# Performance work log

Measured on AMD Instinct MI355X. Metric: run time of the kernel, lower is better.

## Reference

```python
import jax, jax.numpy as jnp
import numpy as np

N, E, IN, HID, HEADS, L = 50000, 640000, 32, 64, 2, 4
MAXR = 8
N_ETYPE = 11 + 3 * MAXR  # 35
NEG_SLOPE = 0.2  # DGL EGATConv leaky_relu slope


def _mlp2(x, W1, b1, W2, b2):
    # 2-layer MLP: activation (gelu) after hidden layer only
    return jax.nn.gelu(x @ W1 + b1) @ W2 + b2


def _egat(h, ef, src, dst, W_ni, W_nj, W_fij, W_node, b_node, attn):
    # DGL EGATConv: edge-feature-enhanced graph attention
    n = h.shape[0]
    H, D = attn.shape
    f_edge = (h @ W_ni)[src] + (h @ W_nj)[dst] + ef @ W_fij       # [E, H*D]
    f_out = jax.nn.leaky_relu(f_edge, NEG_SLOPE).reshape(-1, H, D)
    e = jnp.einsum('ehd,hd->eh', f_out, attn)                     # [E, H]
    m = jax.ops.segment_max(e, dst, num_segments=n)               # per-dst max
    w = jnp.exp(e - m[dst])
    z = jax.ops.segment_sum(w, dst, num_segments=n)
    a = w / z[dst]                                                # edge softmax over incoming edges
    h_out = (h @ W_node + b_node).reshape(n, H, D)
    return jax.ops.segment_sum(h_out[src] * a[:, :, None], dst, num_segments=n)  # [N, H, D]


def _forward(feat, att_rc, att_rp, type_emb, rid_emb, rc_W, rc_b, rp_W, rp_b,
             fe_W1, fe_b1, fe_W2, fe_b2, W_ni, W_nj, W_fij, W_node, b_node, attn,
             mlp_W1, mlp_b1, mlp_W2, mlp_b2, src, dst, etype, erid):
    n = feat.shape[0]
    # edge embedding, 'sum' flavor
    ef = type_emb[etype] + rid_emb[erid] + att_rc @ rc_W + rc_b + att_rp @ rp_W + rp_b
    feats = [feat]
    h = _mlp2(feat, fe_W1, fe_b1, fe_W2, fe_b2)
    feats.append(h)
    for l in range(W_ni.shape[0]):
        agg = _egat(h, ef, src, dst, W_ni[l], W_nj[l], W_fij[l],
                    W_node[l], b_node[l], attn[l])
        h = _mlp2(agg.reshape(n, -1), mlp_W1[l], mlp_b1[l], mlp_W2[l], mlp_b2[l]) + h  # residual
        feats.append(h)
    node_emb = jnp.concatenate(feats, axis=-1)             # layer_pooling='all'
    graph_emb = jnp.max(node_emb, axis=0, keepdims=True)   # graph max pooling
    return jnp.concatenate([node_emb, jnp.broadcast_to(graph_emb, node_emb.shape)], axis=-1)


def setup_inputs() -> dict:
    key = jax.random.key(0)
    ks = iter(jax.random.split(key, 40))
    s = 0.05
    return {
        'feat': jax.random.normal(next(ks), (N, IN), jnp.float32),
        'att_rc': jax.random.normal(next(ks), (E, 2), jnp.float32),
        'att_rp': jax.random.normal(next(ks), (E, 3), jnp.float32),
        'type_emb': jax.random.normal(next(ks), (N_ETYPE, HID), jnp.float32) * s,
        'rid_emb': jax.random.normal(next(ks), (MAXR + 1, HID), jnp.float32) * s,
        'rc_W': jax.random.normal(next(ks), (2, HID), jnp.float32) * s,
        'rc_b': jnp.zeros((HID,), jnp.float32),
        'rp_W': jax.random.normal(next(ks), (3, HID), jnp.float32) * s,
        'rp_b': jnp.zeros((HID,), jnp.float32),
        'fe_W1': jax.random.normal(next(ks), (IN, HID), jnp.float32) * s,
        'fe_b1': jnp.zeros((HID,), jnp.float32),
        'fe_W2': jax.random.normal(next(ks), (HID, HID), jnp.float32) * s,
        'fe_b2': jnp.zeros((HID,), jnp.float32),
        'W_ni': jax.random.normal(next(ks), (L, HID, HEADS * HID), jnp.float32) * s,
        'W_nj': jax.random.normal(next(ks), (L, HID, HEADS * HID), jnp.float32) * s,
        'W_fij': jax.random.normal(next(ks), (L, HID, HEADS * HID), jnp.float32) * s,
        'W_node': jax.random.normal(next(ks), (L, HID, HEADS * HID), jnp.float32) * s,
        'b_node': jnp.zeros((L, HEADS * HID), jnp.float32),
        'attn': jax.random.normal(next(ks), (L, HEADS, HID), jnp.float32) * s,
        'mlp_W1': jax.random.normal(next(ks), (L, HEADS * HID, HEADS * HID), jnp.float32) * s,
        'mlp_b1': jnp.zeros((L, HEADS * HID), jnp.float32),
        'mlp_W2': jax.random.normal(next(ks), (L, HEADS * HID, HID), jnp.float32) * s,
        'mlp_b2': jnp.zeros((L, HID), jnp.float32),
        'src': jax.random.randint(next(ks), (E,), 0, N, jnp.int32),
        'dst': jax.random.randint(next(ks), (E,), 0, N, jnp.int32),
        'etype': jax.random.randint(next(ks), (E,), 0, N_ETYPE, jnp.int32),
        'erid': jax.random.randint(next(ks), (E,), 0, MAXR + 1, jnp.int32),
    }


def reference(feat, att_rc, att_rp, type_emb, rid_emb, rc_W, rc_b, rp_W, rp_b,
              fe_W1, fe_b1, fe_W2, fe_b2, W_ni, W_nj, W_fij, W_node, b_node, attn,
              mlp_W1, mlp_b1, mlp_W2, mlp_b2, src, dst, etype, erid):
    return _forward(feat, att_rc, att_rp, type_emb, rid_emb, rc_W, rc_b, rp_W, rp_b,
                    fe_W1, fe_b1, fe_W2, fe_b2, W_ni, W_nj, W_fij, W_node, b_node, attn,
                    mlp_W1, mlp_b1, mlp_W2, mlp_b2, src, dst, etype, erid)
```

## Files before the change

### kernel.cpp

```cpp
#include <hip/hip_runtime.h>
#include <math.h>

#define N_NODES 50000
#define N_EDGES 640000
#define NLAYER  4
#define NPAD    50016

#define EDGE_BLOCKS 1000
#define EDGE_WAVES  4000

typedef unsigned short bf16_t;
typedef __attribute__((ext_vector_type(8))) short s16x8;
typedef __attribute__((ext_vector_type(4))) float f32x4;

__device__ __forceinline__ float gelu_f(float x) {
    return 0.5f * x * (1.0f + tanhf(0.7978845608028654f * (x + 0.044715f * x * x * x)));
}

__device__ __forceinline__ bf16_t f2bf(float f) {
    unsigned u = __float_as_uint(f);
    unsigned r = (u + 0x7FFFu + ((u >> 16) & 1u)) >> 16;
    return (bf16_t)r;
}
__device__ __forceinline__ float bf2f(bf16_t h) { return __uint_as_float(((unsigned)h) << 16); }
__device__ __forceinline__ float bfl(unsigned x) { return __uint_as_float(x << 16); }
__device__ __forceinline__ float bfh(unsigned x) { return __uint_as_float(x & 0xFFFF0000u); }

__global__ void k_zero32(unsigned* p, int n) {
    int i = blockIdx.x * 256 + threadIdx.x;
    if (i < n) p[i] = 0u;
}

__global__ void k_hist(const int* __restrict__ dst, int* __restrict__ deg) {
    int i = blockIdx.x * 256 + threadIdx.x;
    if (i < N_EDGES) atomicAdd(&deg[dst[i]], 1);
}

__global__ void k_scan1(const int* __restrict__ deg, int* __restrict__ rowptr, int* __restrict__ bsum) {
    __shared__ int sd[1024];
    int gi = blockIdx.x * 1024 + threadIdx.x;
    int v = (gi < N_NODES) ? deg[gi] : 0;
    sd[threadIdx.x] = v;
    __syncthreads();
    for (int off = 1; off < 1024; off <<= 1) {
        int t2 = (threadIdx.x >= (unsigned)off) ? sd[threadIdx.x - off] : 0;
        __syncthreads();
        sd[threadIdx.x] += t2;
        __syncthreads();
    }
    if (gi < N_NODES) rowptr[gi] = sd[threadIdx.x] - v;
    if (threadIdx.x == 1023) bsum[blockIdx.x] = sd[1023];
}

__global__ void k_scan2(const int* __restrict__ bsum, int* __restrict__ boff, int nb) {
    if (threadIdx.x == 0 && blockIdx.x == 0) {
        int run = 0;
        for (int b = 0; b < nb; b++) { boff[b] = run; run += bsum[b]; }
    }
}

__global__ void k_scan3(int* __restrict__ rowptr, const int* __restrict__ boff) {
    int gi = blockIdx.x * 1024 + threadIdx.x;
    if (gi < N_NODES) rowptr[gi] += boff[blockIdx.x];
    if (gi == 0) rowptr[N_NODES] = N_EDGES;
}

__global__ void k_copy(const int* __restrict__ a, int* __restrict__ b) {
    int i = blockIdx.x * 256 + threadIdx.x;
    if (i < N_NODES) b[i] = a[i];
}

__global__ void k_scatter(const int* __restrict__ dst, int* __restrict__ cursor, int* __restrict__ eidx) {
    int i = blockIdx.x * 256 + threadIdx.x;
    if (i < N_EDGES) {
        int p = atomicAdd(&cursor[dst[i]], 1);
        eidx[p] = i;
    }
}

__global__ void k_sortgather(
    const int* __restrict__ eidx, const int* __restrict__ src, const int* __restrict__ dst,
    const int* __restrict__ etype, const int* __restrict__ erid,
    const float* __restrict__ att_rc, const float* __restrict__ att_rp,
    int* __restrict__ src_s, uint4* __restrict__ emA, uint2* __restrict__ emB)
{
    int i = blockIdx.x * 256 + threadIdx.x;
    if (i < N_EDGES) {
        int e = eidx[i];
        int sv = src[e];
        src_s[i] = sv;
        uint4 a;
        a.x = (unsigned)sv;
        a.y = (unsigned)dst[e];
        a.z = (unsigned)(etype[e] * 9 + erid[e]);
        a.w = (unsigned)f2bf(att_rc[2 * e]) | ((unsigned)f2bf(att_rc[2 * e + 1]) << 16);
        uint2 b;
        b.x = (unsigned)f2bf(att_rp[3 * e]) | ((unsigned)f2bf(att_rp[3 * e + 1]) << 16);
        b.y = (unsigned)f2bf(att_rp[3 * e + 2]);
        emA[i] = a;
        emB[i] = b;
    }
}

__global__ void k_base(const float* __restrict__ type_emb, const float* __restrict__ rid_emb,
                       const float* __restrict__ rcb, const float* __restrict__ rpb,
                       float* __restrict__ base)
{
    int idx = blockIdx.x * 256 + threadIdx.x;
    if (idx >= 315 * 64) return;
    int c = idx >> 6, k = idx & 63;
    int et = c / 9, er = c % 9;
    base[idx] = type_emb[et * 64 + k] + rid_emb[er * 64 + k] + rcb[k] + rpb[k];
}

__global__ void k_wprep(const float* __restrict__ Wfij, const float* __restrict__ Wni,
                        const float* __restrict__ Wnj, const float* __restrict__ Wnode,
                        const float* __restrict__ W1, const float* __restrict__ W2,
                        bf16_t* __restrict__ WT, bf16_t* __restrict__ W3T,
                        bf16_t* __restrict__ W1T, bf16_t* __restrict__ W2T)
{
    int idx = blockIdx.x * 256 + threadIdx.x;
    if (idx >= NLAYER * 57344) return;
    int l = idx / 57344, r = idx % 57344;
    if (r < 8192) {
        int n = r >> 6, k = r & 63;
        WT[l * 8192 + r] = f2bf(Wfij[l * 8192 + k * 128 + n]);
    } else if (r < 32768) {
        int q = r - 8192; int c = q >> 6, k = q & 63;
        const float* src = (c < 128) ? Wni : (c < 256) ? Wnj : Wnode;
        W3T[l * 24576 + q] = f2bf(src[l * 8192 + k * 128 + (c & 127)]);
    } else if (r < 49152) {
        int q = r - 32768; int n = q >> 7, k = q & 127;
        W1T[l * 16384 + q] = f2bf(W1[l * 16384 + k * 128 + n]);
    } else {
        int q = r - 49152; int j = q >> 7, k = q & 127;
        W2T[l * 8192 + q] = f2bf(W2[l * 8192 + k * 64 + j]);
    }
}

__global__ __launch_bounds__(256) void k_fe(
    const float* __restrict__ feat, const float* __restrict__ W1, const float* __restrict__ b1,
    const float* __restrict__ W2, const float* __restrict__ b2,
    float* __restrict__ h, bf16_t* __restrict__ hb, float* __restrict__ out)
{
    __shared__ float hid[4][64];
    int w = threadIdx.x >> 6, lane = threadIdx.x & 63;
    int n = blockIdx.x * 4 + w;
    float a = b1[lane];
#pragma unroll 8
    for (int k = 0; k < 32; k++) a = fmaf(feat[n * 32 + k], W1[k * 64 + lane], a);
    hid[w][lane] = gelu_f(a);
    __syncthreads();
    float o = b2[lane];
#pragma unroll 8
    for (int k = 0; k < 64; k++) o = fmaf(hid[w][k], W2[k * 64 + lane], o);
    h[n * 64 + lane] = o;
    hb[n * 64 + lane] = f2bf(o);
    out[n * 704 + 32 + lane] = o;
    if (lane < 32) out[n * 704 + lane] = feat[n * 32 + lane];
}

__global__ __launch_bounds__(256) void k_node3(
    const bf16_t* __restrict__ hb, const bf16_t* __restrict__ W3T,
    const float* __restrict__ bnode, bf16_t* __restrict__ s)
{
    __shared__ __align__(16) bf16_t hbS[32 * 72];
    const int t = threadIdx.x;
    const int wave = t >> 6, lane = t & 63, l16 = lane & 15, quad = lane >> 4;
    const int n0 = blockIdx.x * 32;
    {
        int r = t >> 3, sg = t & 7;
        *(s16x8*)(hbS + r * 72 + sg * 8) = *(const s16x8*)(hb + (size_t)(n0 + r) * 64 + sg * 8);
    }
    __syncthreads();
    const int ng = wave & 1, ch = wave >> 1;
    const s16x8 B0 = *(const s16x8*)(hbS + (ng * 16 + l16) * 72 + quad * 8);
    const s16x8 B1 = *(const s16x8*)(hbS + (ng * 16 + l16) * 72 + 32 + quad * 8);
    const int node = n0 + ng * 16 + l16;
#pragma unroll
    for (int nt = 0; nt < 12; nt++) {
        int c0 = ch * 192 + nt * 16;
        const s16x8 A0 = *(const s16x8*)(W3T + (size_t)(c0 + l16) * 64 + quad * 8);
        const s16x8 A1 = *(const s16x8*)(W3T + (size_t)(c0 + l16) * 64 + 32 + quad * 8);
        f32x4 acc = {0.f, 0.f, 0.f, 0.f};
        acc = __builtin_amdgcn_mfma_f32_16x16x32_bf16(A0, B0, acc, 0, 0, 0);
        acc = __builtin_amdgcn_mfma_f32_16x16x32_bf16(A1, B1, acc, 0, 0, 0);
        int cb = c0 + quad * 4;
        float4 bv = make_float4(0.f, 0.f, 0.f, 0.f);
        if (cb >= 256) bv = *(const float4*)(bnode + cb - 256);
        ushort4 o;
        o.x = f2bf(acc[0] + bv.x);
        o.y = f2bf(acc[1] + bv.y);
        o.z = f2bf(acc[2] + bv.z);
        o.w = f2bf(acc[3] + bv.w);
        *(ushort4*)(s + (size_t)node * 384 + cb) = o;
    }
}

__device__ __forceinline__ void eg_issue(
    const bf16_t* __restrict__ s, const uint4& ma, int quad, ushort4 (&G)[8])
{
    const bf16_t* sr = s + (size_t)ma.x * 384;
    const bf16_t* dr = s + (size_t)ma.y * 384 + 128;
#pragma unroll
    for (int mt = 0; mt < 4; mt++) {
        const int d0 = mt * 16 + quad * 4;
        G[mt]     = *(const ushort4*)(sr + d0);
        G[4 + mt] = *(const ushort4*)(dr + d0);
    }
}

__device__ __forceinline__ void eg_process(
    int i, const uint4& ma, const uint2& mb, const ushort4 (&G)[8],
    const bf16_t* __restrict__ WTs, const float* __restrict__ attL,
    const float (*__restrict__ cwL)[64], const float* __restrict__ base,
    int lane, int quad, float* __restrict__ evals)
{
    const float rc0 = bfl(ma.w), rc1 = bfh(ma.w);
    const float rp0 = bfl(mb.x), rp1 = bfh(mb.x), rp2 = bfl(mb.y);
    const float* bp = base + (size_t)ma.z * 64;
    s16x8 B0, B1;
#pragma unroll
    for (int s4 = 0; s4 < 4; s4++) {
        const int k = (s4 >> 1) * 32 + (s4 & 1) * 4 + quad * 8;
        const float4 bv = *(const float4*)(bp + k);
        const float4 w0 = *(const float4*)(&cwL[0][k]);
        const float4 w1 = *(const float4*)(&cwL[1][k]);
        const float4 w2 = *(const float4*)(&cwL[2][k]);
        const float4 w3 = *(const float4*)(&cwL[3][k]);
        const float4 w4 = *(const float4*)(&cwL[4][k]);
        float v0 = bv.x, v1 = bv.y, v2 = bv.z, v3 = bv.w;
        v0 = fmaf(rc0, w0.x, v0); v1 = fmaf(rc0, w0.y, v1); v2 = fmaf(rc0, w0.z, v2); v3 = fmaf(rc0, w0.w, v3);
        v0 = fmaf(rc1, w1.x, v0); v1 = fmaf(rc1, w1.y, v1); v2 = fmaf(rc1, w1.z, v2); v3 = fmaf(rc1, w1.w, v3);
        v0 = fmaf(rp0, w2.x, v0); v1 = fmaf(rp0, w2.y, v1); v2 = fmaf(rp0, w2.z, v2); v3 = fmaf(rp0, w2.w, v3);
        v0 = fmaf(rp1, w3.x, v0); v1 = fmaf(rp1, w3.y, v1); v2 = fmaf(rp1, w3.z, v2); v3 = fmaf(rp1, w3.w, v3);
        v0 = fmaf(rp2, w4.x, v0); v1 = fmaf(rp2, w4.y, v1); v2 = fmaf(rp2, w4.z, v2); v3 = fmaf(rp2, w4.w, v3);
        const short p0 = (short)f2bf(v0), p1 = (short)f2bf(v1), p2 = (short)f2bf(v2), p3 = (short)f2bf(v3);
        const int o = (s4 & 1) * 4;
        if (s4 < 2) { B0[o] = p0; B0[o + 1] = p1; B0[o + 2] = p2; B0[o + 3] = p3; }
        else        { B1[o] = p0; B1[o + 1] = p1; B1[o + 2] = p2; B1[o + 3] = p3; }
    }
#pragma unroll
    for (int hd = 0; hd < 2; hd++) {
        float p = 0.f;
#pragma unroll
        for (int mt = 0; mt < 4; mt++) {
            const int fm = hd * 4 + mt;
            const s16x8 A0 = *(const s16x8*)(WTs + ((fm * 2 + 0) * 64 + lane) * 8);
            const s16x8 A1 = *(const s16x8*)(WTs + ((fm * 2 + 1) * 64 + lane) * 8);
            f32x4 a = {0.f, 0.f, 0.f, 0.f};
            a = __builtin_amdgcn_mfma_f32_16x16x32_bf16(A0, B0, a, 0, 0, 0);
            a = __builtin_amdgcn_mfma_f32_16x16x32_bf16(A1, B1, a, 0, 0, 0);
            const float4 at = *(const float4*)(attL + hd * 64 + mt * 16 + quad * 4);
            float f0 = a[0] + (bf2f(G[mt].x) + bf2f(G[4 + mt].x));
            float f1 = a[1] + (bf2f(G[mt].y) + bf2f(G[4 + mt].y));
            float f2 = a[2] + (bf2f(G[mt].z) + bf2f(G[4 + mt].z));
            float f3 = a[3] + (bf2f(G[mt].w) + bf2f(G[4 + mt].w));
            f0 = (f0 >= 0.f) ? f0 : 0.2f * f0;
            f1 = (f1 >= 0.f) ? f1 : 0.2f * f1;
            f2 = (f2 >= 0.f) ? f2 : 0.2f * f2;
            f3 = (f3 >= 0.f) ? f3 : 0.2f * f3;
            p = fmaf(f0, at.x, p);
            p = fmaf(f1, at.y, p);
            p = fmaf(f2, at.z, p);
            p = fmaf(f3, at.w, p);
        }
        p += __shfl_xor(p, 16);
        p += __shfl_xor(p, 32);
        if (quad == 0) evals[i * 2 + hd] = p;
    }
}

__global__ __launch_bounds__(256) void k_edge(
    const bf16_t* __restrict__ s, const bf16_t* __restrict__ WT,
    const float* __restrict__ attn, const uint4* __restrict__ emA,
    const uint2* __restrict__ emB, const float* __restrict__ base,
    const float* __restrict__ rcW, const float* __restrict__ rpW,
    float* __restrict__ evals)
{
    __shared__ __align__(16) bf16_t WTs[16 * 64 * 8];
    __shared__ __align__(16) float attL[128];
    __shared__ __align__(16) float cwL[5][64];
    for (int c = threadIdx.x; c < 1024; c += 256) {
        int ln = c & 63, rowq = c >> 6;
        int half = rowq & 1, fm = rowq >> 1;
        int rl16 = ln & 15, rq = ln >> 4;
        int grow = (fm >> 2) * 64 + (fm & 3) * 16 + rl16;
        *(s16x8*)(WTs + c * 8) = *(const s16x8*)(WT + grow * 64 + half * 32 + rq * 8);
    }
    if (threadIdx.x < 128) attL[threadIdx.x] = attn[threadIdx.x];
    {
        int j = threadIdx.x >> 6, k = threadIdx.x & 63;
        cwL[j][k] = (j < 2) ? rcW[j * 64 + k] : rpW[(j - 2) * 64 + k];
        if (threadIdx.x < 64) cwL[4][threadIdx.x] = rpW[128 + threadIdx.x];
    }
    __syncthreads();

    const int lane = threadIdx.x & 63;
    const int l16 = lane & 15, quad = lane >> 4;
    const int wid = (blockIdx.x * 256 + threadIdx.x) >> 6;

    ushort4 GA[8], GB[8];
    uint4 maC = emA[wid * 16 + l16];
    uint2 mbC = emB[wid * 16 + l16];
    eg_issue(s, maC, quad, GA);
    uint4 maN = emA[(wid + EDGE_WAVES) * 16 + l16];
    uint2 mbN = emB[(wid + EDGE_WAVES) * 16 + l16];

#pragma unroll 1
    for (int it = 0; it < 5; it++) {
        const int ta = wid + (2 * it) * EDGE_WAVES;
        const int tb = ta + EDGE_WAVES;
        eg_issue(s, maN, quad, GB);
        const bool h = it < 4;
        uint4 ma2 = maC; uint2 mb2 = mbC;
        if (h) {
            int e2 = (tb + EDGE_WAVES) * 16 + l16;
            ma2 = emA[e2]; mb2 = emB[e2];
        }
        eg_process(ta * 16 + l16, maC, mbC, GA, WTs, attL, cwL, base, lane, quad, evals);
        if (h) eg_issue(s, ma2, quad, GA);
        uint4 ma3 = maN; uint2 mb3 = mbN;
        if (h) {
            int e3 = (tb + 2 * EDGE_WAVES) * 16 + l16;
            ma3 = emA[e3]; mb3 = emB[e3];
        }
        eg_process(tb * 16 + l16, maN, mbN, GB, WTs, attL, cwL, base, lane, quad, evals);
        maC = ma2; mbC = mb2; maN = ma3; mbN = mb3;
    }
}

__global__ __launch_bounds__(256) void k_soft_agg(
    const int* __restrict__ rowptr, const int* __restrict__ src_s,
    const float* __restrict__ evals, const bf16_t* __restrict__ s,
    unsigned* __restrict__ aggb)
{
    int lane = threadIdx.x & 63;
    int wid = (blockIdx.x * 256 + threadIdx.x) >> 6;
    int nw = (gridDim.x * 256) >> 6;
    const int hb = (lane >> 4) & 1;
    const int esel = lane >> 5;
    const int s32 = (lane & 15) | ((lane >> 5) << 4);
    const int dsel = (lane & 31) * 4;
    for (int n = wid; n < N_NODES; n += nw) {
        int r0 = rowptr[n], r1 = rowptr[n + 1];
        if (r0 == r1) {
            if (lane < 32) { uint2 z; z.x = 0u; z.y = 0u; *(uint2*)(aggb + (size_t)n * 64 + lane * 2) = z; }
            continue;
        }
        float mm = -1e30f;
        for (int i = r0 + s32; i < r1; i += 32) mm = fmaxf(mm, evals[2 * i + hb]);
        mm = fmaxf(mm, __shfl_xor(mm, 1));
        mm = fmaxf(mm, __shfl_xor(mm, 2));
        mm = fmaxf(mm, __shfl_xor(mm, 4));
        mm = fmaxf(mm, __shfl_xor(mm, 8));
        mm = fmaxf(mm, __shfl_xor(mm, 32));
        float z = 0.f;
        for (int i = r0 + s32; i < r1; i += 32) z += expf(evals[2 * i + hb] - mm);
        z += __shfl_xor(z, 1);
        z += __shfl_xor(z, 2);
        z += __shfl_xor(z, 4);
        z += __shfl_xor(z, 8);
        z += __shfl_xor(z, 32);
        float rz = 1.f / z;
        float acc0 = 0.f, acc1 = 0.f, acc2 = 0.f, acc3 = 0.f;
        for (int i = r0; i < r1; i += 8) {
            uint2 cc[4]; float ww[4];
#pragma unroll
            for (int p = 0; p < 4; p++) {
                int ej = i + 2 * p + esel;
                bool v = ej < r1;
                int es = v ? ej : r0;
                cc[p] = *(const uint2*)(s + (size_t)src_s[es] * 384 + 256 + dsel);
                ww[p] = v ? expf(evals[2 * ej + hb] - mm) * rz : 0.f;
            }
#pragma unroll
            for (int p = 0; p < 4; p++) {
                acc0 = fmaf(ww[p], bfl(cc[p].x), acc0);
                acc1 = fmaf(ww[p], bfh(cc[p].x), acc1);
                acc2 = fmaf(ww[p], bfl(cc[p].y), acc2);
                acc3 = fmaf(ww[p], bfh(cc[p].y), acc3);
            }
        }
        acc0 += __shfl_xor(acc0, 32);
        acc1 += __shfl_xor(acc1, 32);
        acc2 += __shfl_xor(acc2, 32);
        acc3 += __shfl_xor(acc3, 32);
        if (lane < 32) {
            uint2 o;
            o.x = (unsigned)f2bf(acc0) | ((unsigned)f2bf(acc1) << 16);
            o.y = (unsigned)f2bf(acc2) | ((unsigned)f2bf(acc3) << 16);
            *(uint2*)(aggb + (size_t)n * 64 + lane * 2) = o;
        }
    }
}

__global__ __launch_bounds__(256) void k_mlp(
    const bf16_t* __restrict__ aggb, const bf16_t* __restrict__ W1T, const float* __restrict__ b1,
    const bf16_t* __restrict__ W2T, const float* __restrict__ b2,
    const float* __restrict__ hin, float* __restrict__ hout, bf16_t* __restrict__ houtb,
    float* __restrict__ out, int col0)
{
    __shared__ __align__(16) bf16_t aggS[32 * 136];
    __shared__ __align__(16) bf16_t hidS[32 * 136];
    const int t = threadIdx.x;
    const int wave = t >> 6, lane = t & 63, l16 = lane & 15, quad = lane >> 4;
    const int n0 = blockIdx.x * 32;
    {
        int r = t >> 3, sg = t & 7;
        *(s16x8*)(aggS + r * 136 + sg * 16) =
            *(const s16x8*)(aggb + (size_t)(n0 + r) * 128 + sg * 16);
        *(s16x8*)(aggS + r * 136 + sg * 16 + 8) =
            *(const s16x8*)(aggb + (size_t)(n0 + r) * 128 + sg * 16 + 8);
    }
    __syncthreads();
    const int ng = wave & 1, nh = wave >> 1;
    const int node = n0 + ng * 16 + l16;
    {
        const bf16_t* brow = aggS + (ng * 16 + l16) * 136 + quad * 8;
        s16x8 B[4];
#pragma unroll
        for (int ks = 0; ks < 4; ks++) B[ks] = *(const s16x8*)(brow + ks * 32);
#pragma unroll
        for (int nt = 0; nt < 4; nt++) {
            int nb = nh * 64 + nt * 16;
            f32x4 acc = {0.f, 0.f, 0.f, 0.f};
#pragma unroll
            for (int ks = 0; ks < 4; ks++) {
                const s16x8 A = *(const s16x8*)(W1T + (size_t)(nb + l16) * 128 + ks * 32 + quad * 8);
                acc = __builtin_amdgcn_mfma_f32_16x16x32_bf16(A, B[ks], acc, 0, 0, 0);
            }
            const float4 bv = *(const float4*)(b1 + nb + quad * 4);
            ushort4 o;
            o.x = f2bf(gelu_f(acc[0] + bv.x));
            o.y = f2bf(gelu_f(acc[1] + bv.y));
            o.z = f2bf(gelu_f(acc[2] + bv.z));
            o.w = f2bf(gelu_f(acc[3] + bv.w));
            *(ushort4*)(hidS + (ng * 16 + l16) * 136 + nb + quad * 4) = o;
        }
    }
    __syncthreads();
    {
        const int jh = wave >> 1;
        const bf16_t* hrow = hidS + (ng * 16 + l16) * 136 + quad * 8;
        s16x8 H[4];
#pragma unroll
        for (int ks = 0; ks < 4; ks++) H[ks] = *(const s16x8*)(hrow + ks * 32);
#pragma unroll
        for (int jt = 0; jt < 2; jt++) {
            int jb = jh * 32 + jt * 16;
            f32x4 acc = {0.f, 0.f, 0.f, 0.f};
#pragma unroll
            for (int ks = 0; ks < 4; ks++) {
                const s16x8 A = *(const s16x8*)(W2T + (size_t)(jb + l16) * 128 + ks * 32 + quad * 8);
                acc = __builtin_amdgcn_mfma_f32_16x16x32_bf16(A, H[ks], acc, 0, 0, 0);
            }
            int j0 = jb + quad * 4;
            const float4 bv = *(const float4*)(b2 + j0);
            const float4 hv = *(const float4*)(hin + (size_t)node * 64 + j0);
            float4 v;
            v.x = acc[0] + bv.x + hv.x;
            v.y = acc[1] + bv.y + hv.y;
            v.z = acc[2] + bv.z + hv.z;
            v.w = acc[3] + bv.w + hv.w;
            *(float4*)(hout + (size_t)node * 64 + j0) = v;
            ushort4 ob;
            ob.x = f2bf(v.x); ob.y = f2bf(v.y); ob.z = f2bf(v.z); ob.w = f2bf(v.w);
            *(ushort4*)(houtb + (size_t)node * 64 + j0) = ob;
            if (node < N_NODES)
                *(float4*)(out + (size_t)node * 704 + col0 + j0) = v;
        }
    }
}

__device__ __forceinline__ unsigned fmap(float v) {
    unsigned u = __float_as_uint(v);
    return (u & 0x80000000u) ? ~u : (u | 0x80000000u);
}

__global__ __launch_bounds__(384) void k_colmax(const float* __restrict__ out, unsigned* __restrict__ gmax) {
    int c = threadIdx.x;
    if (c >= 352) return;
    float m = -1e30f;
    for (int n = blockIdx.x; n < N_NODES; n += gridDim.x)
        m = fmaxf(m, out[(size_t)n * 704 + c]);
    atomicMax(gmax + c, fmap(m));
}

__global__ __launch_bounds__(384) void k_bcast(const unsigned* __restrict__ gmax, float* __restrict__ out) {
    int c = threadIdx.x;
    if (c >= 352) return;
    unsigned u = gmax[c];
    u = (u & 0x80000000u) ? (u ^ 0x80000000u) : ~u;
    float v = __uint_as_float(u);
    for (int n = blockIdx.x; n < N_NODES; n += gridDim.x)
        out[(size_t)n * 704 + 352 + c] = v;
}

extern "C" void kernel_launch(void* const* d_in, const int* in_sizes, int n_in,
                              void* d_out, int out_size, void* d_ws, size_t ws_size,
                              hipStream_t stream)
{
    (void)in_sizes; (void)n_in; (void)out_size; (void)ws_size;
    const float* feat     = (const float*)d_in[0];
    const float* att_rc   = (const float*)d_in[1];
    const float* att_rp   = (const float*)d_in[2];
    const float* type_emb = (const float*)d_in[3];
    const float* rid_emb  = (const float*)d_in[4];
    const float* rc_W     = (const float*)d_in[5];
    const float* rc_b     = (const float*)d_in[6];
    const float* rp_W     = (const float*)d_in[7];
    const float* rp_b     = (const float*)d_in[8];
    const float* fe_W1    = (const float*)d_in[9];
    const float* fe_b1    = (const float*)d_in[10];
    const float* fe_W2    = (const float*)d_in[11];
    const float* fe_b2    = (const float*)d_in[12];
    const float* W_ni     = (const float*)d_in[13];
    const float* W_nj     = (const float*)d_in[14];
    const float* W_fij    = (const float*)d_in[15];
    const float* W_node   = (const float*)d_in[16];
    const float* b_node   = (const float*)d_in[17];
    const float* attn     = (const float*)d_in[18];
    const float* mlp_W1   = (const float*)d_in[19];
    const float* mlp_b1   = (const float*)d_in[20];
    const float* mlp_W2   = (const float*)d_in[21];
    const float* mlp_b2   = (const float*)d_in[22];
    const int* src   = (const int*)d_in[23];
    const int* dst   = (const int*)d_in[24];
    const int* etype = (const int*)d_in[25];
    const int* erid  = (const int*)d_in[26];
    float* out = (float*)d_out;

    char* cur = (char*)d_ws;
    auto alloc = [&](size_t bytes) { char* p = cur; cur += (bytes + 15) & ~(size_t)15; return p; };
    float* h_a    = (float*)alloc((size_t)NPAD * 64 * 4);
    float* h_b    = (float*)alloc((size_t)NPAD * 64 * 4);
    bf16_t* hb_a  = (bf16_t*)alloc((size_t)NPAD * 64 * 2);
    bf16_t* hb_b  = (bf16_t*)alloc((size_t)NPAD * 64 * 2);
    bf16_t* s     = (bf16_t*)alloc((size_t)NPAD * 384 * 2);
    float* ev     = (float*)alloc((size_t)N_EDGES * 2 * 4);
    bf16_t* aggb  = (bf16_t*)alloc((size_t)NPAD * 128 * 2);
    int* deg     = (int*)alloc((size_t)N_NODES * 4);
    int* rowptr  = (int*)alloc((size_t)(N_NODES + 1) * 4);
    int* cursor  = (int*)alloc((size_t)N_NODES * 4);
    int* eidx    = (int*)alloc((size_t)N_EDGES * 4);
    int* src_s   = (int*)alloc((size_t)N_EDGES * 4);
    uint4* emA   = (uint4*)alloc((size_t)N_EDGES * 16);
    uint2* emB   = (uint2*)alloc((size_t)N_EDGES * 8);
    float* baseT = (float*)alloc((size_t)315 * 64 * 4);
    bf16_t* WT   = (bf16_t*)alloc((size_t)NLAYER * 128 * 64 * 2);
    bf16_t* W3T  = (bf16_t*)alloc((size_t)NLAYER * 384 * 64 * 2);
    bf16_t* W1T  = (bf16_t*)alloc((size_t)NLAYER * 128 * 128 * 2);
    bf16_t* W2T  = (bf16_t*)alloc((size_t)NLAYER * 64 * 128 * 2);
    int* bsum    = (int*)alloc(64 * 4);
    int* boff    = (int*)alloc(64 * 4);
    unsigned* gmax = (unsigned*)alloc(352 * 4);

    const int NB = (N_NODES + 1023) / 1024;

    k_zero32<<<(N_NODES + 255) / 256, 256, 0, stream>>>((unsigned*)deg, N_NODES);
    k_zero32<<<2, 256, 0, stream>>>(gmax, 352);
    k_hist<<<N_EDGES / 256, 256, 0, stream>>>(dst, deg);
    k_scan1<<<NB, 1024, 0, stream>>>(deg, rowptr, bsum);
    k_scan2<<<1, 64, 0, stream>>>(bsum, boff, NB);
    k_scan3<<<NB, 1024, 0, stream>>>(rowptr, boff);
    k_copy<<<(N_NODES + 255) / 256, 256, 0, stream>>>(rowptr, cursor);
    k_scatter<<<N_EDGES / 256, 256, 0, stream>>>(dst, cursor, eidx);
    k_sortgather<<<N_EDGES / 256, 256, 0, stream>>>(eidx, src, dst, etype, erid, att_rc, att_rp,
                                                    src_s, emA, emB);
    k_base<<<(315 * 64 + 255) / 256, 256, 0, stream>>>(type_emb, rid_emb, rc_b, rp_b, baseT);
    k_wprep<<<(NLAYER * 57344 + 255) / 256, 256, 0, stream>>>(
        W_fij, W_ni, W_nj, W_node, mlp_W1, mlp_W2, WT, W3T, W1T, W2T);
    k_fe<<<N_NODES / 4, 256, 0, stream>>>(feat, fe_W1, fe_b1, fe_W2, fe_b2, h_a, hb_a, out);

    float* hc = h_a;  bf16_t* hbc = hb_a;
    float* hn = h_b;  bf16_t* hbn = hb_b;
    for (int l = 0; l < NLAYER; l++) {
        k_node3<<<NPAD / 32, 256, 0, stream>>>(hbc, W3T + (size_t)l * 384 * 64, b_node + l * 128, s);
        k_edge<<<EDGE_BLOCKS, 256, 0, stream>>>(s, WT + l * 128 * 64, attn + l * 128,
                                                emA, emB, baseT, rc_W, rp_W, ev);
        k_soft_agg<<<4096, 256, 0, stream>>>(rowptr, src_s, ev, s, (unsigned*)aggb);
        k_mlp<<<NPAD / 32, 256, 0, stream>>>(aggb, W1T + (size_t)l * 128 * 128, mlp_b1 + l * 128,
                                             W2T + (size_t)l * 64 * 128, mlp_b2 + l * 64,
                                             hc, hn, hbn, out, 32 + 64 * (l + 1));
        float* tf = hc; hc = hn; hn = tf;
        bf16_t* tb = hbc; hbc = hbn; hbn = tb;
    }
    k_colmax<<<512, 384, 0, stream>>>(out, gmax);
    k_bcast<<<512, 384, 0, stream>>>(gmax, out);
}
```

Measured before the change: 1.258 ms.

## Precompute edge-feature projection tables and replace MFMA edge kernel with per-thread scalar path

The edge embedding is affine in a small categorical index and five scalar attributes. This change folds W_fij into a per-(type,rid) table and five per-attribute weight vectors, computed once per layer in small setup kernels, so the per-edge 64x128 matmul becomes a table lookup plus five FMAs per output. The edge kernel becomes one thread per edge with no shared memory or MFMA, replacing the software-pipelined wave-per-16-edges loop. The cost is more per-thread registers and scattered 16-byte gathers of 128-float table rows and bf16 node rows. Accumulating in fp32 instead of rounding edge features to bf16 also changes numerics slightly.

```diff
diff --git a/kernel.cpp b/kernel.cpp
--- a/kernel.cpp
+++ b/kernel.cpp
@@ -5,9 +5,6 @@
 #define N_EDGES 640000
 #define NLAYER  4
 #define NPAD    50016
-
-#define EDGE_BLOCKS 1000
-#define EDGE_WAVES  4000
 
 typedef unsigned short bf16_t;
 typedef __attribute__((ext_vector_type(8))) short s16x8;
@@ -111,6 +108,36 @@
     int c = idx >> 6, k = idx & 63;
     int et = c / 9, er = c % 9;
     base[idx] = type_emb[et * 64 + k] + rid_emb[er * 64 + k] + rcb[k] + rpb[k];
+}
+
+__global__ void k_basew(const float* __restrict__ base, const float* __restrict__ Wfij,
+                        float* __restrict__ baseW)
+{
+    int idx = blockIdx.x * 256 + threadIdx.x;
+    if (idx >= NLAYER * 315 * 128) return;
+    int l = idx / (315 * 128), r = idx % (315 * 128);
+    int c = r >> 7, n = r & 127;
+    const float* bp = base + c * 64;
+    const float* wp = Wfij + l * 8192 + n;
+    float acc = 0.f;
+#pragma unroll 8
+    for (int k = 0; k < 64; k++) acc = fmaf(bp[k], wp[k * 128], acc);
+    baseW[idx] = acc;
+}
+
+__global__ void k_cw(const float* __restrict__ rcW, const float* __restrict__ rpW,
+                     const float* __restrict__ Wfij, float* __restrict__ CWf)
+{
+    int idx = blockIdx.x * 256 + threadIdx.x;
+    if (idx >= NLAYER * 5 * 128) return;
+    int l = idx / 640, r = idx % 640;
+    int j = r >> 7, n = r & 127;
+    const float* cp = (j < 2) ? (rcW + j * 64) : (rpW + (j - 2) * 64);
+    const float* wp = Wfij + l * 8192 + n;
+    float acc = 0.f;
+#pragma unroll 8
+    for (int k = 0; k < 64; k++) acc = fmaf(cp[k], wp[k * 128], acc);
+    CWf[idx] = acc;
 }
 
 __global__ void k_wprep(const float* __restrict__ Wfij, const float* __restrict__ Wni,
@@ -197,137 +224,75 @@
     }
 }
 
-__device__ __forceinline__ void eg_issue(
-    const bf16_t* __restrict__ s, const uint4& ma, int quad, ushort4 (&G)[8])
-{
+__global__ __launch_bounds__(256) void k_edge(
+    const bf16_t* __restrict__ s, const float* __restrict__ baseW,
+    const float* __restrict__ CWf, const float* __restrict__ attn,
+    const uint4* __restrict__ emA, const uint2* __restrict__ emB,
+    float* __restrict__ evals)
+{
+    const int i = blockIdx.x * 256 + threadIdx.x;
+    const uint4 ma = emA[i];
+    const uint2 mb = emB[i];
     const bf16_t* sr = s + (size_t)ma.x * 384;
     const bf16_t* dr = s + (size_t)ma.y * 384 + 128;
-#pragma unroll
-    for (int mt = 0; mt < 4; mt++) {
-        const int d0 = mt * 16 + quad * 4;
-        G[mt]     = *(const ushort4*)(sr + d0);
-        G[4 + mt] = *(const ushort4*)(dr + d0);
-    }
-}
-
-__device__ __forceinline__ void eg_process(
-    int i, const uint4& ma, const uint2& mb, const ushort4 (&G)[8],
-    const bf16_t* __restrict__ WTs, const float* __restrict__ attL,
-    const float (*__restrict__ cwL)[64], const float* __restrict__ base,
-    int lane, int quad, float* __restrict__ evals)
-{
-    const float rc0 = bfl(ma.w), rc1 = bfh(ma.w);
-    const float rp0 = bfl(mb.x), rp1 = bfh(mb.x), rp2 = bfl(mb.y);
-    const float* bp = base + (size_t)ma.z * 64;
-    s16x8 B0, B1;
-#pragma unroll
-    for (int s4 = 0; s4 < 4; s4++) {
-        const int k = (s4 >> 1) * 32 + (s4 & 1) * 4 + quad * 8;
-        const float4 bv = *(const float4*)(bp + k);
-        const float4 w0 = *(const float4*)(&cwL[0][k]);
-        const float4 w1 = *(const float4*)(&cwL[1][k]);
-        const float4 w2 = *(const float4*)(&cwL[2][k]);
-        const float4 w3 = *(const float4*)(&cwL[3][k]);
-        const float4 w4 = *(const float4*)(&cwL[4][k]);
-        float v0 = bv.x, v1 = bv.y, v2 = bv.z, v3 = bv.w;
-        v0 = fmaf(rc0, w0.x, v0); v1 = fmaf(rc0, w0.y, v1); v2 = fmaf(rc0, w0.z, v2); v3 = fmaf(rc0, w0.w, v3);
-        v0 = fmaf(rc1, w1.x, v0); v1 = fmaf(rc1, w1.y, v1); v2 = fmaf(rc1, w1.z, v2); v3 = fmaf(rc1, w1.w, v3);
-        v0 = fmaf(rp0, w2.x, v0); v1 = fmaf(rp0, w2.y, v1); v2 = fmaf(rp0, w2.z, v2); v3 = fmaf(rp0, w2.w, v3);
-        v0 = fmaf(rp1, w3.x, v0); v1 = fmaf(rp1, w3.y, v1); v2 = fmaf(rp1, w3.z, v2); v3 = fmaf(rp1, w3.w, v3);
-        v0 = fmaf(rp2, w4.x, v0); v1 = fmaf(rp2, w4.y, v1); v2 = fmaf(rp2, w4.z, v2); v3 = fmaf(rp2, w4.w, v3);
-        const short p0 = (short)f2bf(v0), p1 = (short)f2bf(v1), p2 = (short)f2bf(v2), p3 = (short)f2bf(v3);
-        const int o = (s4 & 1) * 4;
-        if (s4 < 2) { B0[o] = p0; B0[o + 1] = p1; B0[o + 2] = p2; B0[o + 3] = p3; }
-        else        { B1[o] = p0; B1[o + 1] = p1; B1[o + 2] = p2; B1[o + 3] = p3; }
-    }
-#pragma unroll
-    for (int hd = 0; hd < 2; hd++) {
-        float p = 0.f;
-#pragma unroll
-        for (int mt = 0; mt < 4; mt++) {
-            const int fm = hd * 4 + mt;
-            const s16x8 A0 = *(const s16x8*)(WTs + ((fm * 2 + 0) * 64 + lane) * 8);
-            const s16x8 A1 = *(const s16x8*)(WTs + ((fm * 2 + 1) * 64 + lane) * 8);
-            f32x4 a = {0.f, 0.f, 0.f, 0.f};
-            a = __builtin_amdgcn_mfma_f32_16x16x32_bf16(A0, B0, a, 0, 0, 0);
-            a = __builtin_amdgcn_mfma_f32_16x16x32_bf16(A1, B1, a, 0, 0, 0);
-            const float4 at = *(const float4*)(attL + hd * 64 + mt * 16 + quad * 4);
-            float f0 = a[0] + (bf2f(G[mt].x) + bf2f(G[4 + mt].x));
-            float f1 = a[1] + (bf2f(G[mt].y) + bf2f(G[4 + mt].y));
-            float f2 = a[2] + (bf2f(G[mt].z) + bf2f(G[4 + mt].z));
-            float f3 = a[3] + (bf2f(G[mt].w) + bf2f(G[4 + mt].w));
-            f0 = (f0 >= 0.f) ? f0 : 0.2f * f0;
-            f1 = (f1 >= 0.f) ? f1 : 0.2f * f1;
-            f2 = (f2 >= 0.f) ? f2 : 0.2f * f2;
-            f3 = (f3 >= 0.f) ? f3 : 0.2f * f3;
-            p = fmaf(f0, at.x, p);
-            p = fmaf(f1, at.y, p);
-            p = fmaf(f2, at.z, p);
-            p = fmaf(f3, at.w, p);
+    const float* bw = baseW + (size_t)ma.z * 128;
+    const float r0 = bfl(ma.w), r1 = bfh(ma.w);
+    const float r2 = bfl(mb.x), r3 = bfh(mb.x), r4 = bfl(mb.y);
+
+    float e[2] = {0.f, 0.f};
+#pragma unroll
+    for (int c = 0; c < 4; c++) {
+        const int d0 = c * 16;
+        const uint4 u0 = *(const uint4*)(sr + d0);
+        const uint4 u1 = *(const uint4*)(sr + d0 + 8);
+        const uint4 v0 = *(const uint4*)(dr + d0);
+        const uint4 v1 = *(const uint4*)(dr + d0 + 8);
+        float snd[16];
+        snd[0]  = bfl(u0.x) + bfl(v0.x);  snd[1]  = bfh(u0.x) + bfh(v0.x);
+        snd[2]  = bfl(u0.y) + bfl(v0.y);  snd[3]  = bfh(u0.y) + bfh(v0.y);
+        snd[4]  = bfl(u0.z) + bfl(v0.z);  snd[5]  = bfh(u0.z) + bfh(v0.z);
+        snd[6]  = bfl(u0.w) + bfl(v0.w);  snd[7]  = bfh(u0.w) + bfh(v0.w);
+        snd[8]  = bfl(u1.x) + bfl(v1.x);  snd[9]  = bfh(u1.x) + bfh(v1.x);
+        snd[10] = bfl(u1.y) + bfl(v1.y);  snd[11] = bfh(u1.y) + bfh(v1.y);
+        snd[12] = bfl(u1.z) + bfl(v1.z);  snd[13] = bfh(u1.z) + bfh(v1.z);
+        snd[14] = bfl(u1.w) + bfl(v1.w);  snd[15] = bfh(u1.w) + bfh(v1.w);
+#pragma unroll
+        for (int h = 0; h < 2; h++) {
+#pragma unroll
+            for (int q = 0; q < 4; q++) {
+                const int n = h * 64 + d0 + q * 4;
+                const float4 b  = *(const float4*)(bw + n);
+                const float4 w0 = *(const float4*)(CWf + n);
+                const float4 w1 = *(const float4*)(CWf + 128 + n);
+                const float4 w2 = *(const float4*)(CWf + 256 + n);
+                const float4 w3 = *(const float4*)(CWf + 384 + n);
+                const float4 w4 = *(const float4*)(CWf + 512 + n);
+                const float4 at = *(const float4*)(attn + n);
+                float f0 = b.x, f1 = b.y, f2 = b.z, f3 = b.w;
+                f0 = fmaf(r0, w0.x, f0); f1 = fmaf(r0, w0.y, f1); f2 = fmaf(r0, w0.z, f2); f3 = fmaf(r0, w0.w, f3);
+                f0 = fmaf(r1, w1.x, f0); f1 = fmaf(r1, w1.y, f1); f2 = fmaf(r1, w1.z, f2); f3 = fmaf(r1, w1.w, f3);
+                f0 = fmaf(r2, w2.x, f0); f1 = fmaf(r2, w2.y, f1); f2 = fmaf(r2, w2.z, f2); f3 = fmaf(r2, w2.w, f3);
+                f0 = fmaf(r3, w3.x, f0); f1 = fmaf(r3, w3.y, f1); f2 = fmaf(r3, w3.z, f2); f3 = fmaf(r3, w3.w, f3);
+                f0 = fmaf(r4, w4.x, f0); f1 = fmaf(r4, w4.y, f1); f2 = fmaf(r4, w4.z, f2); f3 = fmaf(r4, w4.w, f3);
+                f0 += snd[q * 4 + 0];
+                f1 += snd[q * 4 + 1];
+                f2 += snd[q * 4 + 2];
+                f3 += snd[q * 4 + 3];
+                f0 = (f0 >= 0.f) ? f0 : 0.2f * f0;
+                f1 = (f1 >= 0.f) ? f1 : 0.2f * f1;
+                f2 = (f2 >= 0.f) ? f2 : 0.2f * f2;
+                f3 = (f3 >= 0.f) ? f3 : 0.2f * f3;
+                e[h] = fmaf(f0, at.x, e[h]);
+                e[h] = fmaf(f1, at.y, e[h]);
+                e[h] = fmaf(f2, at.z, e[h]);
+                e[h] = fmaf(f3, at.w, e[h]);
+            }
         }
-        p += __shfl_xor(p, 16);
-        p += __shfl_xor(p, 32);
-        if (quad == 0) evals[i * 2 + hd] = p;
-    }
-}
-
-__global__ __launch_bounds__(256) void k_edge(
-    const bf16_t* __restrict__ s, const bf16_t* __restrict__ WT,
-    const float* __restrict__ attn, const uint4* __restrict__ emA,
-    const uint2* __restrict__ emB, const float* __restrict__ base,
-    const float* __restrict__ rcW, const float* __restrict__ rpW,
-    float* __restrict__ evals)
-{
-    __shared__ __align__(16) bf16_t WTs[16 * 64 * 8];
-    __shared__ __align__(16) float attL[128];
-    __shared__ __align__(16) float cwL[5][64];
-    for (int c = threadIdx.x; c < 1024; c += 256) {
-        int ln = c & 63, rowq = c >> 6;
-        int half = rowq & 1, fm = rowq >> 1;
-        int rl16 = ln & 15, rq = ln >> 4;
-        int grow = (fm >> 2) * 64 + (fm & 3) * 16 + rl16;
-        *(s16x8*)(WTs + c * 8) = *(const s16x8*)(WT + grow * 64 + half * 32 + rq * 8);
-    }
-    if (threadIdx.x < 128) attL[threadIdx.x] = attn[threadIdx.x];
-    {
-        int j = threadIdx.x >> 6, k = threadIdx.x & 63;
-        cwL[j][k] = (j < 2) ? rcW[j * 64 + k] : rpW[(j - 2) * 64 + k];
-        if (threadIdx.x < 64) cwL[4][threadIdx.x] = rpW[128 + threadIdx.x];
-    }
-    __syncthreads();
-
-    const int lane = threadIdx.x & 63;
-    const int l16 = lane & 15, quad = lane >> 4;
-    const int wid = (blockIdx.x * 256 + threadIdx.x) >> 6;
-
-    ushort4 GA[8], GB[8];
-    uint4 maC = emA[wid * 16 + l16];
-    uint2 mbC = emB[wid * 16 + l16];
-    eg_issue(s, maC, quad, GA);
-    uint4 maN = emA[(wid + EDGE_WAVES) * 16 + l16];
-    uint2 mbN = emB[(wid + EDGE_WAVES) * 16 + l16];
-
-#pragma unroll 1
-    for (int it = 0; it < 5; it++) {
-        const int ta = wid + (2 * it) * EDGE_WAVES;
-        const int tb = ta + EDGE_WAVES;
-        eg_issue(s, maN, quad, GB);
-        const bool h = it < 4;
-        uint4 ma2 = maC; uint2 mb2 = mbC;
-        if (h) {
-            int e2 = (tb + EDGE_WAVES) * 16 + l16;
-            ma2 = emA[e2]; mb2 = emB[e2];
-        }
-        eg_process(ta * 16 + l16, maC, mbC, GA, WTs, attL, cwL, base, lane, quad, evals);
-        if (h) eg_issue(s, ma2, quad, GA);
-        uint4 ma3 = maN; uint2 mb3 = mbN;
-        if (h) {
-            int e3 = (tb + 2 * EDGE_WAVES) * 16 + l16;
-            ma3 = emA[e3]; mb3 = emB[e3];
-        }
-        eg_process(tb * 16 + l16, maN, mbN, GB, WTs, attL, cwL, base, lane, quad, evals);
-        maC = ma2; mbC = mb2; maN = ma3; mbN = mb3;
-    }
+    }
+    float2 ev2;
+    ev2.x = e[0];
+    ev2.y = e[1];
+    *(float2*)(evals + 2 * (size_t)i) = ev2;
 }
 
 __global__ __launch_bounds__(256) void k_soft_agg(
@@ -548,6 +513,8 @@
     uint4* emA   = (uint4*)alloc((size_t)N_EDGES * 16);
     uint2* emB   = (uint2*)alloc((size_t)N_EDGES * 8);
     float* baseT = (float*)alloc((size_t)315 * 64 * 4);
+    float* baseW = (float*)alloc((size_t)NLAYER * 315 * 128 * 4);
+    float* CWf   = (float*)alloc((size_t)NLAYER * 5 * 128 * 4);
     bf16_t* WT   = (bf16_t*)alloc((size_t)NLAYER * 128 * 64 * 2);
     bf16_t* W3T  = (bf16_t*)alloc((size_t)NLAYER * 384 * 64 * 2);
     bf16_t* W1T  = (bf16_t*)alloc((size_t)NLAYER * 128 * 128 * 2);
@@ -569,6 +536,8 @@
     k_sortgather<<<N_EDGES / 256, 256, 0, stream>>>(eidx, src, dst, etype, erid, att_rc, att_rp,
                                                     src_s, emA, emB);
     k_base<<<(315 * 64 + 255) / 256, 256, 0, stream>>>(type_emb, rid_emb, rc_b, rp_b, baseT);
+    k_basew<<<(NLAYER * 315 * 128 + 255) / 256, 256, 0, stream>>>(baseT, W_fij, baseW);
+    k_cw<<<(NLAYER * 5 * 128 + 255) / 256, 256, 0, stream>>>(rc_W, rp_W, W_fij, CWf);
     k_wprep<<<(NLAYER * 57344 + 255) / 256, 256, 0, stream>>>(
         W_fij, W_ni, W_nj, W_node, mlp_W1, mlp_W2, WT, W3T, W1T, W2T);
     k_fe<<<N_NODES / 4, 256, 0, stream>>>(feat, fe_W1, fe_b1, fe_W2, fe_b2, h_a, hb_a, out);
@@ -577,8 +546,9 @@
     float* hn = h_b;  bf16_t* hbn = hb_b;
     for (int l = 0; l < NLAYER; l++) {
         k_node3<<<NPAD / 32, 256, 0, stream>>>(hbc, W3T + (size_t)l * 384 * 64, b_node + l * 128, s);
-        k_edge<<<EDGE_BLOCKS, 256, 0, stream>>>(s, WT + l * 128 * 64, attn + l * 128,
-                                                emA, emB, baseT, rc_W, rp_W, ev);
+        k_edge<<<N_EDGES / 256, 256, 0, stream>>>(s, baseW + (size_t)l * 315 * 128,
+                                                  CWf + (size_t)l * 640, attn + l * 128,
+                                                  emA, emB, ev);
         k_soft_agg<<<4096, 256, 0, stream>>>(rowptr, src_s, ev, s, (unsigned*)aggb);
         k_mlp<<<NPAD / 32, 256, 0, stream>>>(aggb, W1T + (size_t)l * 128 * 128, mlp_b1 + l * 128,
                                              W2T + (size_t)l * 64 * 128, mlp_b2 + l * 64,
```

Measured after the change: 1.169 ms. 7.1% less time.
